# Kernel optimization log

Measured on AMD Instinct MI355X. Metric: run time of the kernel, lower is better.

The kernel has to match this reference:

```python
import jax, jax.numpy as jnp
import numpy as np

B, IN, H, OUT = 32768, 64, 256, 768
HM, TS = 4, 64  # hm_modalities, timestep_size; OUT = 3*HM*TS


def setup_inputs() -> dict:
    key = jax.random.key(0)
    ks = jax.random.split(key, 24)
    def w(k, shape):
        scale = 1.0 / np.sqrt(shape[0])
        return jax.random.normal(k, shape, jnp.float32) * scale
    inp = jax.random.normal(ks[0], (B, IN), jnp.float32)
    state1 = jax.random.normal(ks[1], (B, 2 * H), jnp.float32)
    state2 = jax.random.normal(ks[2], (B, 2 * H), jnp.float32)
    d = {"inp": inp, "state1": state1, "state2": state2}
    names = ["wf", "wk", "wi", "ws"]
    for i, n in enumerate(names):
        d[f"l1_{n}"] = w(ks[3 + i], (IN + H, H))
        d[f"l1_b{n[1]}"] = jnp.zeros((H,), jnp.float32)
        d[f"l2_{n}"] = w(ks[7 + i], (H + H, H))
        d[f"l2_b{n[1]}"] = jnp.zeros((H,), jnp.float32)
    d["ff_w"] = w(ks[11], (H, OUT))
    return d


def lstm_cell(state, x_in, wf, bf, wk, bk, wi, bi, ws, bs):
    h = wf.shape[1]
    prev_out = state[:, :h]
    cell = state[:, h:]
    x = jnp.concatenate([x_in, prev_out], axis=1)
    reset = jax.nn.sigmoid(x @ wf + bf)
    write = jax.nn.sigmoid(x @ wk + bk)
    interm = jnp.tanh(x @ wi + bi)
    read = jax.nn.sigmoid(x @ ws + bs)
    cell = reset * cell + write * interm
    out = read * jnp.tanh(cell)
    return out, jnp.concatenate([out, cell], axis=1)


def reference(inp, state1, state2,
              l1_wf, l1_bf, l1_wk, l1_bk, l1_wi, l1_bi, l1_ws, l1_bs,
              l2_wf, l2_bf, l2_wk, l2_bk, l2_wi, l2_bi, l2_ws, l2_bs,
              ff_w):
    out, new_state1 = lstm_cell(state1, inp, l1_wf, l1_bf, l1_wk, l1_bk,
                                l1_wi, l1_bi, l1_ws, l1_bs)
    out, new_state2 = lstm_cell(state2, out, l2_wf, l2_bf, l2_wk, l2_bk,
                                l2_wi, l2_bi, l2_ws, l2_bs)
    out = out @ ff_w  # [B, OUT]
    third = OUT // 3
    means = out[:, :third]
    deviances = jnp.exp(out[:, third:2 * third])
    mult = out[:, -third:].reshape(B, HM, TS)
    mult = jax.nn.softmax(mult, axis=1).reshape(B, HM * TS)
    return means, deviances, mult, new_state1, new_state2
```

## Files before the change

### kernel.cpp

```cpp
#include <hip/hip_runtime.h>
#include <hip/hip_bf16.h>


typedef __attribute__((ext_vector_type(8))) short short8;
typedef __attribute__((ext_vector_type(4))) short short4_t;
typedef __attribute__((ext_vector_type(4))) float floatx4;

#define BATCH 32768

static const size_t DEV_OFF  = (size_t)BATCH * 256;
static const size_t MULT_OFF = (size_t)2 * BATCH * 256;
static const size_t NS1_OFF  = (size_t)3 * BATCH * 256;
static const size_t NS2_OFF  = NS1_OFF + (size_t)BATCH * 512;

__device__ __forceinline__ unsigned short f2bf(float f) {
    union { float f; unsigned int i; } v; v.f = f;
    unsigned int i = v.i;
    i += 0x7fff + ((i >> 16) & 1);
    return (unsigned short)(i >> 16);
}
__device__ __forceinline__ float sigmoidf_(float x) {
    return 1.f / (1.f + __expf(-x));
}

#define W1P_ELEMS (4 * 256 * 320)
#define W2P_ELEMS (4 * 256 * 512)
#define W3P_ELEMS (768 * 256)

__global__ void pack_w(
    const float* __restrict__ a0, const float* __restrict__ a1,
    const float* __restrict__ a2, const float* __restrict__ a3,
    const float* __restrict__ c0, const float* __restrict__ c1,
    const float* __restrict__ c2, const float* __restrict__ c3,
    const float* __restrict__ fw,
    unsigned short* __restrict__ dst)
{
    int idx = blockIdx.x * 256 + threadIdx.x;
    if (idx < W1P_ELEMS) {
        int g = idx / (256 * 320), rem = idx % (256 * 320);
        int n = rem / 320, k = rem % 320;
        const float* s = g == 0 ? a0 : g == 1 ? a1 : g == 2 ? a2 : a3;
        dst[idx] = f2bf(s[k * 256 + n]);
    } else if (idx < W1P_ELEMS + W2P_ELEMS) {
        int j = idx - W1P_ELEMS;
        int g = j / (256 * 512), rem = j % (256 * 512);
        int n = rem / 512, k = rem % 512;
        const float* s = g == 0 ? c0 : g == 1 ? c1 : g == 2 ? c2 : c3;
        dst[idx] = f2bf(s[k * 256 + n]);
    } else {
        int j = idx - (W1P_ELEMS + W2P_ELEMS);
        int n = j / 256, k = j % 256;
        dst[idx] = f2bf(fw[k * 768 + n]);
    }
}

template<int KTOT>
__global__ __launch_bounds__(256) void lstm_layer_k(
    const float* __restrict__ x0, int x0_stride, int x0_cols,
    const float* __restrict__ state,
    const unsigned short* __restrict__ wp,
    const float* __restrict__ bias0, const float* __restrict__ bias1,
    const float* __restrict__ bias2, const float* __restrict__ bias3,
    float* __restrict__ nstate)
{
    __shared__ __align__(16) union {
        struct {
            unsigned short xs[64][72];
            unsigned short ws[4][64][72];
        } st;
        float s[64][260];
    } lds;

    const int tid  = threadIdx.x;
    const int wave = tid >> 6;
    const int lane = tid & 63;
    const int lhi  = lane >> 4, llo = lane & 15;
    const int row0 = blockIdx.x * 64;
    const int jt   = blockIdx.y * 64;

    floatx4 acc[4][4];
#pragma unroll
    for (int i = 0; i < 4; i++)
#pragma unroll
        for (int j = 0; j < 4; j++) acc[i][j] = (floatx4){0.f, 0.f, 0.f, 0.f};

    for (int c = 0; c < KTOT / 64; ++c) {
        const int kbase = c * 64;
        {
            const float* src; int scol, sstr;
            if (kbase < x0_cols) { src = x0;   scol = kbase;           sstr = x0_stride; }
            else                 { src = state; scol = kbase - x0_cols; sstr = 512; }
            const int l4 = tid & 15; const int r0 = tid >> 4;
#pragma unroll
            for (int p = 0; p < 4; ++p) {
                int r = r0 + p * 16;
                float4 v = *(const float4*)(src + (size_t)(row0 + r) * sstr + scol + l4 * 4);
                short4_t h;
                h.x = (short)f2bf(v.x); h.y = (short)f2bf(v.y);
                h.z = (short)f2bf(v.z); h.w = (short)f2bf(v.w);
                *(short4_t*)&lds.st.xs[r][l4 * 4] = h;
            }
        }
        {
            const int l8 = lane & 7, nr = lane >> 3;
            const unsigned short* wsrc = wp + ((size_t)wave * 256 + jt) * KTOT + kbase;
#pragma unroll
            for (int p = 0; p < 8; ++p) {
                int n = p * 8 + nr;
                *(uint4*)&lds.st.ws[wave][n][l8 * 8] =
                    *(const uint4*)(wsrc + (size_t)n * KTOT + l8 * 8);
            }
        }
        __syncthreads();
#pragma unroll
        for (int ks = 0; ks < 2; ++ks) {
            const int k8 = ks * 32 + lhi * 8;
            short8 a[4], b[4];
#pragma unroll
            for (int mi = 0; mi < 4; mi++)
                a[mi] = *(const short8*)&lds.st.xs[mi * 16 + llo][k8];
#pragma unroll
            for (int ni = 0; ni < 4; ni++)
                b[ni] = *(const short8*)&lds.st.ws[wave][ni * 16 + llo][k8];
#pragma unroll
            for (int mi = 0; mi < 4; mi++)
#pragma unroll
                for (int ni = 0; ni < 4; ni++)
                    acc[mi][ni] = __builtin_amdgcn_mfma_f32_16x16x32_bf16(
                        a[mi], b[ni], acc[mi][ni], 0, 0, 0);
        }
        __syncthreads();
    }

    {
        const float* bp = wave == 0 ? bias0 : wave == 1 ? bias1
                        : wave == 2 ? bias2 : bias3;
#pragma unroll
        for (int ni = 0; ni < 4; ni++) {
            float bv = bp[jt + ni * 16 + llo];
#pragma unroll
            for (int mi = 0; mi < 4; mi++)
#pragma unroll
                for (int r = 0; r < 4; r++) {
                    int m = mi * 16 + lhi * 4 + r;
                    lds.s[m][wave * 64 + ni * 16 + llo] = acc[mi][ni][r] + bv;
                }
        }
    }
    __syncthreads();

    for (int it = 0; it < 16; ++it) {
        int e = tid + it * 256;
        int r = e >> 6, h = e & 63;
        float zf = lds.s[r][h];
        float zk = lds.s[r][64 + h];
        float zi = lds.s[r][128 + h];
        float zs = lds.s[r][192 + h];
        float rst = sigmoidf_(zf);
        float wrt = sigmoidf_(zk);
        float itm = tanhf(zi);
        float rd  = sigmoidf_(zs);
        size_t rowel = (size_t)(row0 + r) * 512;
        float cold = state[rowel + 256 + jt + h];
        float cell = rst * cold + wrt * itm;
        float o = rd * tanhf(cell);
        nstate[rowel + jt + h]       = o;
        nstate[rowel + 256 + jt + h] = cell;
    }
}

__global__ __launch_bounds__(256) void ff_k(
    const float* __restrict__ x,
    const unsigned short* __restrict__ wp,
    float* __restrict__ out)
{
    __shared__ __align__(16) union {
        struct {
            unsigned short xs[64][72];
            unsigned short ws[4][64][72];
        } st;
        float s[64][260];
    } lds;

    const int tid  = threadIdx.x;
    const int wave = tid >> 6;
    const int lane = tid & 63;
    const int lhi  = lane >> 4, llo = lane & 15;
    const int row0  = blockIdx.x * 64;
    const int ncol0 = blockIdx.y * 256;

    floatx4 acc[4][4];
#pragma unroll
    for (int i = 0; i < 4; i++)
#pragma unroll
        for (int j = 0; j < 4; j++) acc[i][j] = (floatx4){0.f, 0.f, 0.f, 0.f};

    for (int c = 0; c < 4; ++c) {
        const int kbase = c * 64;
        {
            const int l4 = tid & 15; const int r0 = tid >> 4;
#pragma unroll
            for (int p = 0; p < 4; ++p) {
                int r = r0 + p * 16;
                float4 v = *(const float4*)(x + (size_t)(row0 + r) * 512 + kbase + l4 * 4);
                short4_t h;
                h.x = (short)f2bf(v.x); h.y = (short)f2bf(v.y);
                h.z = (short)f2bf(v.z); h.w = (short)f2bf(v.w);
                *(short4_t*)&lds.st.xs[r][l4 * 4] = h;
            }
        }
        {
            const int l8 = lane & 7, nr = lane >> 3;
            const unsigned short* wsrc = wp + (size_t)(ncol0 + wave * 64) * 256 + kbase;
#pragma unroll
            for (int p = 0; p < 8; ++p) {
                int n = p * 8 + nr;
                *(uint4*)&lds.st.ws[wave][n][l8 * 8] =
                    *(const uint4*)(wsrc + (size_t)n * 256 + l8 * 8);
            }
        }
        __syncthreads();
#pragma unroll
        for (int ks = 0; ks < 2; ++ks) {
            const int k8 = ks * 32 + lhi * 8;
            short8 a[4], b[4];
#pragma unroll
            for (int mi = 0; mi < 4; mi++)
                a[mi] = *(const short8*)&lds.st.xs[mi * 16 + llo][k8];
#pragma unroll
            for (int ni = 0; ni < 4; ni++)
                b[ni] = *(const short8*)&lds.st.ws[wave][ni * 16 + llo][k8];
#pragma unroll
            for (int mi = 0; mi < 4; mi++)
#pragma unroll
                for (int ni = 0; ni < 4; ni++)
                    acc[mi][ni] = __builtin_amdgcn_mfma_f32_16x16x32_bf16(
                        a[mi], b[ni], acc[mi][ni], 0, 0, 0);
        }
        __syncthreads();
    }

    if (blockIdx.y < 2) {
        const size_t obase = (blockIdx.y == 0) ? (size_t)0 : DEV_OFF;
        const bool doexp = (blockIdx.y == 1);
#pragma unroll
        for (int mi = 0; mi < 4; mi++)
#pragma unroll
            for (int ni = 0; ni < 4; ni++) {
                int cc = wave * 64 + ni * 16 + llo;
#pragma unroll
                for (int r = 0; r < 4; r++) {
                    int m = mi * 16 + lhi * 4 + r;
                    float v = acc[mi][ni][r];
                    if (doexp) v = __expf(v);
                    out[obase + (size_t)(row0 + m) * 256 + cc] = v;
                }
            }
    } else {
#pragma unroll
        for (int mi = 0; mi < 4; mi++)
#pragma unroll
            for (int ni = 0; ni < 4; ni++)
#pragma unroll
                for (int r = 0; r < 4; r++) {
                    int m = mi * 16 + lhi * 4 + r;
                    lds.s[m][wave * 64 + ni * 16 + llo] = acc[mi][ni][r];
                }
        __syncthreads();
        for (int it = 0; it < 16; ++it) {
            int e = tid + it * 256;
            int r = e >> 6, t = e & 63;
            float v0 = lds.s[r][t];
            float v1 = lds.s[r][64 + t];
            float v2 = lds.s[r][128 + t];
            float v3 = lds.s[r][192 + t];
            float mx = fmaxf(fmaxf(v0, v1), fmaxf(v2, v3));
            float e0 = __expf(v0 - mx), e1 = __expf(v1 - mx);
            float e2 = __expf(v2 - mx), e3 = __expf(v3 - mx);
            float inv = 1.f / (e0 + e1 + e2 + e3);
            size_t base = MULT_OFF + (size_t)(row0 + r) * 256 + t;
            out[base]       = e0 * inv;
            out[base + 64]  = e1 * inv;
            out[base + 128] = e2 * inv;
            out[base + 192] = e3 * inv;
        }
    }
}

extern "C" void kernel_launch(void* const* d_in, const int* in_sizes, int n_in,
                              void* d_out, int out_size, void* d_ws, size_t ws_size,
                              hipStream_t stream)
{
    typedef const float* cfp;
    cfp inp = (cfp)d_in[0];
    cfp st1 = (cfp)d_in[1];
    cfp st2 = (cfp)d_in[2];
    cfp l1w0 = (cfp)d_in[3],  l1w1 = (cfp)d_in[7],  l1w2 = (cfp)d_in[11], l1w3 = (cfp)d_in[15];
    cfp l1b0 = (cfp)d_in[4],  l1b1 = (cfp)d_in[8],  l1b2 = (cfp)d_in[12], l1b3 = (cfp)d_in[16];
    cfp l2w0 = (cfp)d_in[5],  l2w1 = (cfp)d_in[9],  l2w2 = (cfp)d_in[13], l2w3 = (cfp)d_in[17];
    cfp l2b0 = (cfp)d_in[6],  l2b1 = (cfp)d_in[10], l2b2 = (cfp)d_in[14], l2b3 = (cfp)d_in[18];
    cfp ffw = (cfp)d_in[19];

    float* out = (float*)d_out;
    unsigned short* ws = (unsigned short*)d_ws;

    const size_t W1P = 0;
    const size_t W2P = W1P + W1P_ELEMS;
    const size_t W3P = W2P + W2P_ELEMS;

    pack_w<<<4096, 256, 0, stream>>>(l1w0, l1w1, l1w2, l1w3,
                                     l2w0, l2w1, l2w2, l2w3, ffw, ws);

    lstm_layer_k<320><<<dim3(512, 4), 256, 0, stream>>>(
        inp, 64, 64, st1, ws + W1P, l1b0, l1b1, l1b2, l1b3, out + NS1_OFF);

    lstm_layer_k<512><<<dim3(512, 4), 256, 0, stream>>>(
        out + NS1_OFF, 512, 256, st2, ws + W2P, l2b0, l2b1, l2b2, l2b3,
        out + NS2_OFF);

    ff_k<<<dim3(512, 3), 256, 0, stream>>>(out + NS2_OFF, ws + W3P, out);
}
```

Baseline: 556.8 us.

## Pre-convert activations to bf16, interleave gate weights, use 128x128 tiles with direct-to-LDS loads

Activations and states are converted to bf16 once into a workspace, and each LSTM layer's epilogue writes the bf16 hidden output straight into the next GEMM's input buffer. The GEMMs no longer convert fp32 to bf16 on load. Gate weights are interleaved per hidden unit so one 128-column tile holds all four gates for 32 units, and the FF weights are permuted so the softmax groups sit together. Kernels use 128x128 tiles with global_load_lds DMA and a fast exp-based tanh. The cost is an extra pack pass over the input and states, plus unpadded LDS rows that may cause bank conflicts.

```diff
diff --git a/kernel.cpp b/kernel.cpp
--- a/kernel.cpp
+++ b/kernel.cpp
@@ -1,5 +1,4 @@
 #include <hip/hip_runtime.h>
-#include <hip/hip_bf16.h>
 
 
 typedef __attribute__((ext_vector_type(8))) short short8;
@@ -12,6 +11,13 @@
 static const size_t MULT_OFF = (size_t)2 * BATCH * 256;
 static const size_t NS1_OFF  = (size_t)3 * BATCH * 256;
 static const size_t NS2_OFF  = NS1_OFF + (size_t)BATCH * 512;
+
+static const size_t W1P = 0;
+static const size_t W2P = (size_t)1024 * 320;
+static const size_t W3P = W2P + (size_t)1024 * 512;
+static const size_t X1O = W3P + (size_t)768 * 256;
+static const size_t X2O = X1O + (size_t)BATCH * 320;
+static const size_t X3O = X2O + (size_t)BATCH * 512;
 
 __device__ __forceinline__ unsigned short f2bf(float f) {
     union { float f; unsigned int i; } v; v.f = f;
@@ -22,61 +28,118 @@
 __device__ __forceinline__ float sigmoidf_(float x) {
     return 1.f / (1.f + __expf(-x));
 }
-
-#define W1P_ELEMS (4 * 256 * 320)
-#define W2P_ELEMS (4 * 256 * 512)
-#define W3P_ELEMS (768 * 256)
-
-__global__ void pack_w(
-    const float* __restrict__ a0, const float* __restrict__ a1,
-    const float* __restrict__ a2, const float* __restrict__ a3,
-    const float* __restrict__ c0, const float* __restrict__ c1,
-    const float* __restrict__ c2, const float* __restrict__ c3,
-    const float* __restrict__ fw,
-    unsigned short* __restrict__ dst)
+__device__ __forceinline__ float tanhf_(float x) {
+    float e = __expf(2.f * x);
+    return 1.f - 2.f / (e + 1.f);
+}
+
+__device__ __forceinline__ void gl_lds16(const unsigned short* g,
+                                         unsigned short* l) {
+    __builtin_amdgcn_global_load_lds(
+        (const __attribute__((address_space(1))) unsigned int*)g,
+        (__attribute__((address_space(3))) unsigned int*)l,
+        16, 0, 0);
+}
+
+__global__ __launch_bounds__(256) void pack_all(
+    const float* __restrict__ inp, const float* __restrict__ s1,
+    const float* __restrict__ s2,
+    const float* __restrict__ w10, const float* __restrict__ w11,
+    const float* __restrict__ w12, const float* __restrict__ w13,
+    const float* __restrict__ w20, const float* __restrict__ w21,
+    const float* __restrict__ w22, const float* __restrict__ w23,
+    const float* __restrict__ fw, unsigned short* __restrict__ ws)
 {
-    int idx = blockIdx.x * 256 + threadIdx.x;
-    if (idx < W1P_ELEMS) {
-        int g = idx / (256 * 320), rem = idx % (256 * 320);
-        int n = rem / 320, k = rem % 320;
-        const float* s = g == 0 ? a0 : g == 1 ? a1 : g == 2 ? a2 : a3;
-        dst[idx] = f2bf(s[k * 256 + n]);
-    } else if (idx < W1P_ELEMS + W2P_ELEMS) {
-        int j = idx - W1P_ELEMS;
-        int g = j / (256 * 512), rem = j % (256 * 512);
-        int n = rem / 512, k = rem % 512;
-        const float* s = g == 0 ? c0 : g == 1 ? c1 : g == 2 ? c2 : c3;
-        dst[idx] = f2bf(s[k * 256 + n]);
+    const int q = blockIdx.x * 256 + threadIdx.x;
+    if (q < 524288) {
+        int r = q >> 4, c = (q & 15) << 2;
+        float4 v = *(const float4*)(inp + (size_t)r * 64 + c);
+        short4_t h;
+        h.x = (short)f2bf(v.x); h.y = (short)f2bf(v.y);
+        h.z = (short)f2bf(v.z); h.w = (short)f2bf(v.w);
+        *(short4_t*)(ws + X1O + (size_t)r * 320 + c) = h;
+    } else if (q < 2621440) {
+        int j = q - 524288;
+        int r = j >> 6, c = (j & 63) << 2;
+        float4 v = *(const float4*)(s1 + (size_t)r * 512 + c);
+        short4_t h;
+        h.x = (short)f2bf(v.x); h.y = (short)f2bf(v.y);
+        h.z = (short)f2bf(v.z); h.w = (short)f2bf(v.w);
+        *(short4_t*)(ws + X1O + (size_t)r * 320 + 64 + c) = h;
+    } else if (q < 4718592) {
+        int j = q - 2621440;
+        int r = j >> 6, c = (j & 63) << 2;
+        float4 v = *(const float4*)(s2 + (size_t)r * 512 + c);
+        short4_t h;
+        h.x = (short)f2bf(v.x); h.y = (short)f2bf(v.y);
+        h.z = (short)f2bf(v.z); h.w = (short)f2bf(v.w);
+        *(short4_t*)(ws + X2O + (size_t)r * 512 + 256 + c) = h;
+    } else if (q < 4800512) {
+        int j = q - 4718592;
+        int n = j / 80, k = (j % 80) << 2;
+        int h = n >> 2, g = n & 3;
+        const float* s = g == 0 ? w10 : g == 1 ? w11 : g == 2 ? w12 : w13;
+        short4_t o;
+        o.x = (short)f2bf(s[(size_t)(k + 0) * 256 + h]);
+        o.y = (short)f2bf(s[(size_t)(k + 1) * 256 + h]);
+        o.z = (short)f2bf(s[(size_t)(k + 2) * 256 + h]);
+        o.w = (short)f2bf(s[(size_t)(k + 3) * 256 + h]);
+        *(short4_t*)(ws + W1P + (size_t)n * 320 + k) = o;
+    } else if (q < 4931584) {
+        int j = q - 4800512;
+        int n = j >> 7, k = (j & 127) << 2;
+        int h = n >> 2, g = n & 3;
+        const float* s = g == 0 ? w20 : g == 1 ? w21 : g == 2 ? w22 : w23;
+        short4_t o;
+        o.x = (short)f2bf(s[(size_t)(k + 0) * 256 + h]);
+        o.y = (short)f2bf(s[(size_t)(k + 1) * 256 + h]);
+        o.z = (short)f2bf(s[(size_t)(k + 2) * 256 + h]);
+        o.w = (short)f2bf(s[(size_t)(k + 3) * 256 + h]);
+        *(short4_t*)(ws + W2P + (size_t)n * 512 + k) = o;
     } else {
-        int j = idx - (W1P_ELEMS + W2P_ELEMS);
-        int n = j / 256, k = j % 256;
-        dst[idx] = f2bf(fw[k * 768 + n]);
-    }
-}
-
-template<int KTOT>
-__global__ __launch_bounds__(256) void lstm_layer_k(
-    const float* __restrict__ x0, int x0_stride, int x0_cols,
+        int j = q - 4931584;
+        int n = j >> 6, k = (j & 63) << 2;
+        int col = (n < 512) ? n : (512 + ((n & 3) << 6) + ((n - 512) >> 2));
+        short4_t o;
+        o.x = (short)f2bf(fw[(size_t)(k + 0) * 768 + col]);
+        o.y = (short)f2bf(fw[(size_t)(k + 1) * 768 + col]);
+        o.z = (short)f2bf(fw[(size_t)(k + 2) * 768 + col]);
+        o.w = (short)f2bf(fw[(size_t)(k + 3) * 768 + col]);
+        *(short4_t*)(ws + W3P + (size_t)n * 256 + k) = o;
+    }
+}
+
+template<int KT, int XST>
+__global__ __launch_bounds__(256) void lstm_gemm(
+    const unsigned short* __restrict__ xin,
+    const unsigned short* __restrict__ wp,
+    const float* __restrict__ b0, const float* __restrict__ b1,
+    const float* __restrict__ b2, const float* __restrict__ b3,
     const float* __restrict__ state,
-    const unsigned short* __restrict__ wp,
-    const float* __restrict__ bias0, const float* __restrict__ bias1,
-    const float* __restrict__ bias2, const float* __restrict__ bias3,
-    float* __restrict__ nstate)
+    float* __restrict__ nstate,
+    unsigned short* __restrict__ xnext)
 {
     __shared__ __align__(16) union {
-        struct {
-            unsigned short xs[64][72];
-            unsigned short ws[4][64][72];
-        } st;
-        float s[64][260];
+        struct { unsigned short a[128][64]; unsigned short b[128][64]; } st;
+        float ep[128][68];
     } lds;
+    __shared__ float sbias[4][32];
 
     const int tid  = threadIdx.x;
-    const int wave = tid >> 6;
+    const int w    = tid >> 6;
     const int lane = tid & 63;
     const int lhi  = lane >> 4, llo = lane & 15;
-    const int row0 = blockIdx.x * 64;
-    const int jt   = blockIdx.y * 64;
+    const int wr   = w >> 1, wc = w & 1;
+    const int nt   = blockIdx.x;
+    const int row0 = blockIdx.y * 128;
+    const int nc0  = nt * 128;
+    const int hbase = nt * 32;
+
+    if (tid < 128) {
+        int g = tid >> 5, hl = tid & 31;
+        const float* bp = g == 0 ? b0 : g == 1 ? b1 : g == 2 ? b2 : b3;
+        sbias[g][hl] = bp[hbase + hl];
+    }
 
     floatx4 acc[4][4];
 #pragma unroll
@@ -84,32 +147,19 @@
 #pragma unroll
         for (int j = 0; j < 4; j++) acc[i][j] = (floatx4){0.f, 0.f, 0.f, 0.f};
 
-    for (int c = 0; c < KTOT / 64; ++c) {
-        const int kbase = c * 64;
-        {
-            const float* src; int scol, sstr;
-            if (kbase < x0_cols) { src = x0;   scol = kbase;           sstr = x0_stride; }
-            else                 { src = state; scol = kbase - x0_cols; sstr = 512; }
-            const int l4 = tid & 15; const int r0 = tid >> 4;
-#pragma unroll
-            for (int p = 0; p < 4; ++p) {
-                int r = r0 + p * 16;
-                float4 v = *(const float4*)(src + (size_t)(row0 + r) * sstr + scol + l4 * 4);
-                short4_t h;
-                h.x = (short)f2bf(v.x); h.y = (short)f2bf(v.y);
-                h.z = (short)f2bf(v.z); h.w = (short)f2bf(v.w);
-                *(short4_t*)&lds.st.xs[r][l4 * 4] = h;
-            }
-        }
-        {
-            const int l8 = lane & 7, nr = lane >> 3;
-            const unsigned short* wsrc = wp + ((size_t)wave * 256 + jt) * KTOT + kbase;
-#pragma unroll
-            for (int p = 0; p < 8; ++p) {
-                int n = p * 8 + nr;
-                *(uint4*)&lds.st.ws[wave][n][l8 * 8] =
-                    *(const uint4*)(wsrc + (size_t)n * KTOT + l8 * 8);
-            }
+    const int arow  = (w << 5) + (lane >> 3);
+    const int acolb = (lane & 7) << 3;
+    const unsigned short* agp = xin + (size_t)(row0 + arow) * KT + acolb;
+    const unsigned short* bgp = wp  + (size_t)(nc0 + arow) * KT + acolb;
+
+    for (int c = 0; c < KT / 64; ++c) {
+        const int kb = c << 6;
+#pragma unroll
+        for (int p = 0; p < 4; ++p) {
+            gl_lds16(agp + (size_t)(p * 8) * KT + kb,
+                     &lds.st.a[(w << 5) + (p << 3)][0]);
+            gl_lds16(bgp + (size_t)(p * 8) * KT + kb,
+                     &lds.st.b[(w << 5) + (p << 3)][0]);
         }
         __syncthreads();
 #pragma unroll
@@ -118,10 +168,10 @@
             short8 a[4], b[4];
 #pragma unroll
             for (int mi = 0; mi < 4; mi++)
-                a[mi] = *(const short8*)&lds.st.xs[mi * 16 + llo][k8];
+                a[mi] = *(const short8*)&lds.st.a[wr * 64 + mi * 16 + llo][k8];
 #pragma unroll
             for (int ni = 0; ni < 4; ni++)
-                b[ni] = *(const short8*)&lds.st.ws[wave][ni * 16 + llo][k8];
+                b[ni] = *(const short8*)&lds.st.b[wc * 64 + ni * 16 + llo][k8];
 #pragma unroll
             for (int mi = 0; mi < 4; mi++)
 #pragma unroll
@@ -132,62 +182,61 @@
         __syncthreads();
     }
 
-    {
-        const float* bp = wave == 0 ? bias0 : wave == 1 ? bias1
-                        : wave == 2 ? bias2 : bias3;
-#pragma unroll
-        for (int ni = 0; ni < 4; ni++) {
-            float bv = bp[jt + ni * 16 + llo];
-#pragma unroll
-            for (int mi = 0; mi < 4; mi++)
-#pragma unroll
-                for (int r = 0; r < 4; r++) {
-                    int m = mi * 16 + lhi * 4 + r;
-                    lds.s[m][wave * 64 + ni * 16 + llo] = acc[mi][ni][r] + bv;
-                }
-        }
-    }
-    __syncthreads();
-
-    for (int it = 0; it < 16; ++it) {
-        int e = tid + it * 256;
-        int r = e >> 6, h = e & 63;
-        float zf = lds.s[r][h];
-        float zk = lds.s[r][64 + h];
-        float zi = lds.s[r][128 + h];
-        float zs = lds.s[r][192 + h];
-        float rst = sigmoidf_(zf);
-        float wrt = sigmoidf_(zk);
-        float itm = tanhf(zi);
-        float rd  = sigmoidf_(zs);
-        size_t rowel = (size_t)(row0 + r) * 512;
-        float cold = state[rowel + 256 + jt + h];
-        float cell = rst * cold + wrt * itm;
-        float o = rd * tanhf(cell);
-        nstate[rowel + jt + h]       = o;
-        nstate[rowel + 256 + jt + h] = cell;
-    }
-}
-
-__global__ __launch_bounds__(256) void ff_k(
-    const float* __restrict__ x,
+    for (int pass = 0; pass < 2; ++pass) {
+        if (pass) __syncthreads();
+        if (wc == pass) {
+#pragma unroll
+            for (int mi = 0; mi < 4; mi++)
+#pragma unroll
+                for (int ni = 0; ni < 4; ni++)
+#pragma unroll
+                    for (int r = 0; r < 4; r++)
+                        lds.ep[wr * 64 + mi * 16 + lhi * 4 + r]
+                              [ni * 16 + llo] = acc[mi][ni][r];
+        }
+        __syncthreads();
+        const int hl   = tid & 15;
+        const int hblk = pass * 16 + hl;
+        const int hg   = hbase + hblk;
+        const float bf_ = sbias[0][hblk], bk_ = sbias[1][hblk];
+        const float bi_ = sbias[2][hblk], bs_ = sbias[3][hblk];
+#pragma unroll
+        for (int rr = 0; rr < 8; ++rr) {
+            const int r = (tid >> 4) + rr * 16;
+            float4 z = *(const float4*)&lds.ep[r][hl << 2];
+            float rst = sigmoidf_(z.x + bf_);
+            float wrt = sigmoidf_(z.y + bk_);
+            float itm = tanhf_(z.z + bi_);
+            float rd  = sigmoidf_(z.w + bs_);
+            const size_t rowel = (size_t)(row0 + r) * 512;
+            float cold = state[rowel + 256 + hg];
+            float cell = rst * cold + wrt * itm;
+            float o = rd * tanhf_(cell);
+            nstate[rowel + hg]       = o;
+            nstate[rowel + 256 + hg] = cell;
+            xnext[(size_t)(row0 + r) * XST + hg] = f2bf(o);
+        }
+    }
+}
+
+__global__ __launch_bounds__(256) void ff_gemm(
+    const unsigned short* __restrict__ xin,
     const unsigned short* __restrict__ wp,
     float* __restrict__ out)
 {
     __shared__ __align__(16) union {
-        struct {
-            unsigned short xs[64][72];
-            unsigned short ws[4][64][72];
-        } st;
-        float s[64][260];
+        struct { unsigned short a[128][64]; unsigned short b[128][64]; } st;
+        float ep[128][68];
     } lds;
 
     const int tid  = threadIdx.x;
-    const int wave = tid >> 6;
+    const int w    = tid >> 6;
     const int lane = tid & 63;
     const int lhi  = lane >> 4, llo = lane & 15;
-    const int row0  = blockIdx.x * 64;
-    const int ncol0 = blockIdx.y * 256;
+    const int wr   = w >> 1, wc = w & 1;
+    const int nt   = blockIdx.x;
+    const int row0 = blockIdx.y * 128;
+    const int nc0  = nt * 128;
 
     floatx4 acc[4][4];
 #pragma unroll
@@ -195,29 +244,19 @@
 #pragma unroll
         for (int j = 0; j < 4; j++) acc[i][j] = (floatx4){0.f, 0.f, 0.f, 0.f};
 
+    const int arow  = (w << 5) + (lane >> 3);
+    const int acolb = (lane & 7) << 3;
+    const unsigned short* agp = xin + (size_t)(row0 + arow) * 256 + acolb;
+    const unsigned short* bgp = wp  + (size_t)(nc0 + arow) * 256 + acolb;
+
     for (int c = 0; c < 4; ++c) {
-        const int kbase = c * 64;
-        {
-            const int l4 = tid & 15; const int r0 = tid >> 4;
-#pragma unroll
-            for (int p = 0; p < 4; ++p) {
-                int r = r0 + p * 16;
-                float4 v = *(const float4*)(x + (size_t)(row0 + r) * 512 + kbase + l4 * 4);
-                short4_t h;
-                h.x = (short)f2bf(v.x); h.y = (short)f2bf(v.y);
-                h.z = (short)f2bf(v.z); h.w = (short)f2bf(v.w);
-                *(short4_t*)&lds.st.xs[r][l4 * 4] = h;
-            }
-        }
-        {
-            const int l8 = lane & 7, nr = lane >> 3;
-            const unsigned short* wsrc = wp + (size_t)(ncol0 + wave * 64) * 256 + kbase;
-#pragma unroll
-            for (int p = 0; p < 8; ++p) {
-                int n = p * 8 + nr;
-                *(uint4*)&lds.st.ws[wave][n][l8 * 8] =
-                    *(const uint4*)(wsrc + (size_t)n * 256 + l8 * 8);
-            }
+        const int kb = c << 6;
+#pragma unroll
+        for (int p = 0; p < 4; ++p) {
+            gl_lds16(agp + (size_t)(p * 8) * 256 + kb,
+                     &lds.st.a[(w << 5) + (p << 3)][0]);
+            gl_lds16(bgp + (size_t)(p * 8) * 256 + kb,
+                     &lds.st.b[(w << 5) + (p << 3)][0]);
         }
         __syncthreads();
 #pragma unroll
@@ -226,10 +265,10 @@
             short8 a[4], b[4];
 #pragma unroll
             for (int mi = 0; mi < 4; mi++)
-                a[mi] = *(const short8*)&lds.st.xs[mi * 16 + llo][k8];
+                a[mi] = *(const short8*)&lds.st.a[wr * 64 + mi * 16 + llo][k8];
 #pragma unroll
             for (int ni = 0; ni < 4; ni++)
-                b[ni] = *(const short8*)&lds.st.ws[wave][ni * 16 + llo][k8];
+                b[ni] = *(const short8*)&lds.st.b[wc * 64 + ni * 16 + llo][k8];
 #pragma unroll
             for (int mi = 0; mi < 4; mi++)
 #pragma unroll
@@ -240,49 +279,54 @@
         __syncthreads();
     }
 
-    if (blockIdx.y < 2) {
-        const size_t obase = (blockIdx.y == 0) ? (size_t)0 : DEV_OFF;
-        const bool doexp = (blockIdx.y == 1);
+    if (nt < 4) {
+        const bool dev = (nt >= 2);
+        float* obase = out + (dev ? DEV_OFF : (size_t)0);
+        const int cb = (nt & 1) * 128 + wc * 64;
 #pragma unroll
         for (int mi = 0; mi < 4; mi++)
 #pragma unroll
             for (int ni = 0; ni < 4; ni++) {
-                int cc = wave * 64 + ni * 16 + llo;
+                const int cc = cb + ni * 16 + llo;
 #pragma unroll
                 for (int r = 0; r < 4; r++) {
-                    int m = mi * 16 + lhi * 4 + r;
+                    const int m = wr * 64 + mi * 16 + lhi * 4 + r;
                     float v = acc[mi][ni][r];
-                    if (doexp) v = __expf(v);
-                    out[obase + (size_t)(row0 + m) * 256 + cc] = v;
+                    if (dev) v = __expf(v);
+                    obase[(size_t)(row0 + m) * 256 + cc] = v;
                 }
             }
     } else {
-#pragma unroll
-        for (int mi = 0; mi < 4; mi++)
-#pragma unroll
-            for (int ni = 0; ni < 4; ni++)
-#pragma unroll
-                for (int r = 0; r < 4; r++) {
-                    int m = mi * 16 + lhi * 4 + r;
-                    lds.s[m][wave * 64 + ni * 16 + llo] = acc[mi][ni][r];
-                }
-        __syncthreads();
-        for (int it = 0; it < 16; ++it) {
-            int e = tid + it * 256;
-            int r = e >> 6, t = e & 63;
-            float v0 = lds.s[r][t];
-            float v1 = lds.s[r][64 + t];
-            float v2 = lds.s[r][128 + t];
-            float v3 = lds.s[r][192 + t];
-            float mx = fmaxf(fmaxf(v0, v1), fmaxf(v2, v3));
-            float e0 = __expf(v0 - mx), e1 = __expf(v1 - mx);
-            float e2 = __expf(v2 - mx), e3 = __expf(v3 - mx);
-            float inv = 1.f / (e0 + e1 + e2 + e3);
-            size_t base = MULT_OFF + (size_t)(row0 + r) * 256 + t;
-            out[base]       = e0 * inv;
-            out[base + 64]  = e1 * inv;
-            out[base + 128] = e2 * inv;
-            out[base + 192] = e3 * inv;
+        const int tb = (nt - 4) * 32;
+        for (int pass = 0; pass < 2; ++pass) {
+            if (pass) __syncthreads();
+            if (wc == pass) {
+#pragma unroll
+                for (int mi = 0; mi < 4; mi++)
+#pragma unroll
+                    for (int ni = 0; ni < 4; ni++)
+#pragma unroll
+                        for (int r = 0; r < 4; r++)
+                            lds.ep[wr * 64 + mi * 16 + lhi * 4 + r]
+                                  [ni * 16 + llo] = acc[mi][ni][r];
+            }
+            __syncthreads();
+            const int tl = tid & 15;
+#pragma unroll
+            for (int rr = 0; rr < 8; ++rr) {
+                const int r = (tid >> 4) + rr * 16;
+                float4 z = *(const float4*)&lds.ep[r][tl << 2];
+                float mx = fmaxf(fmaxf(z.x, z.y), fmaxf(z.z, z.w));
+                float e0 = __expf(z.x - mx), e1 = __expf(z.y - mx);
+                float e2 = __expf(z.z - mx), e3 = __expf(z.w - mx);
+                float inv = 1.f / (e0 + e1 + e2 + e3);
+                size_t base = MULT_OFF + (size_t)(row0 + r) * 256
+                            + tb + pass * 16 + tl;
+                out[base]       = e0 * inv;
+                out[base + 64]  = e1 * inv;
+                out[base + 128] = e2 * inv;
+                out[base + 192] = e3 * inv;
+            }
         }
     }
 }
@@ -304,19 +348,17 @@
     float* out = (float*)d_out;
     unsigned short* ws = (unsigned short*)d_ws;
 
-    const size_t W1P = 0;
-    const size_t W2P = W1P + W1P_ELEMS;
-    const size_t W3P = W2P + W2P_ELEMS;
-
-    pack_w<<<4096, 256, 0, stream>>>(l1w0, l1w1, l1w2, l1w3,
-                                     l2w0, l2w1, l2w2, l2w3, ffw, ws);
-
-    lstm_layer_k<320><<<dim3(512, 4), 256, 0, stream>>>(
-        inp, 64, 64, st1, ws + W1P, l1b0, l1b1, l1b2, l1b3, out + NS1_OFF);
-
-    lstm_layer_k<512><<<dim3(512, 4), 256, 0, stream>>>(
-        out + NS1_OFF, 512, 256, st2, ws + W2P, l2b0, l2b1, l2b2, l2b3,
-        out + NS2_OFF);
-
-    ff_k<<<dim3(512, 3), 256, 0, stream>>>(out + NS2_OFF, ws + W3P, out);
-}
+    pack_all<<<19456, 256, 0, stream>>>(inp, st1, st2,
+                                        l1w0, l1w1, l1w2, l1w3,
+                                        l2w0, l2w1, l2w2, l2w3, ffw, ws);
+
+    lstm_gemm<320, 512><<<dim3(8, 256), 256, 0, stream>>>(
+        ws + X1O, ws + W1P, l1b0, l1b1, l1b2, l1b3,
+        st1, out + NS1_OFF, ws + X2O);
+
+    lstm_gemm<512, 256><<<dim3(8, 256), 256, 0, stream>>>(
+        ws + X2O, ws + W2P, l2b0, l2b1, l2b2, l2b3,
+        st2, out + NS2_OFF, ws + X3O);
+
+    ff_gemm<<<dim3(6, 256), 256, 0, stream>>>(ws + X3O, ws + W3P, out);
+}
```

Result: faster. 518.1 us (-6.9%).
